# Kernel tuning notes

Measured on AMD Instinct MI355X. Metric: run time of the kernel, lower is better.

Reference implementation:

```python
import jax, jax.numpy as jnp
import numpy as np

OUTCOMES = [8, 8, 8, 8, 8, 8]           # concept outcome counts (concepts_order)
N_TOTAL = int(np.prod(OUTCOMES))        # 262144 joint states
N_VALID = 8192                          # admissible states
B, D = 4096, 1024


def setup_inputs() -> dict:
    key = jax.random.key(0)
    k1, k2 = jax.random.split(key)
    embeddings = jax.random.normal(k1, (B, D), dtype=jnp.float32)
    W = jax.random.normal(k2, (N_VALID, D), dtype=jnp.float32) * 0.02
    b = jnp.zeros((N_VALID,), dtype=jnp.float32)
    # unique sorted admissible-state indices, like torch.argwhere(mask)
    rng = np.random.default_rng(0)
    valid_states = jnp.asarray(
        np.sort(rng.choice(N_TOTAL, size=N_VALID, replace=False)).astype(np.int32))
    return {"embeddings": embeddings, "W": W, "b": b, "valid_states": valid_states}


def reference(embeddings, W, b, valid_states):
    # softmax over valid states: [B, N_VALID]
    probs = jax.nn.softmax(embeddings @ W.T + b, axis=1)
    probs_t = probs.T  # [N_VALID, B] for leading-axis segment reduction
    marginals = []
    stride = N_TOTAL
    for n_i in OUTCOMES:
        stride //= n_i
        # digit of each valid joint-state index along this concept's axis
        digit = (valid_states // stride) % n_i  # [N_VALID]
        # equivalent to scattering probs into the full joint tensor and
        # summing over all other concept axes, without materializing it
        m = jax.ops.segment_sum(probs_t, digit, num_segments=n_i).T  # [B, n_i]
        marginals.append(m)
    return jnp.stack(marginals)  # [n_concepts, B, 8]
```

## Files before the change

kernel.cpp:

```cpp
#include <hip/hip_runtime.h>
#include <hip/hip_bf16.h>
#include <cstdint>
#include <cstddef>

typedef __bf16 bf16_t;
typedef bf16_t bf16x8 __attribute__((ext_vector_type(8)));
typedef bf16_t bf16x4 __attribute__((ext_vector_type(4)));
typedef float  f32x4  __attribute__((ext_vector_type(4)));
typedef unsigned int u32;

#define BROWS 4096
#define NV    8192
#define KD    1024
#define NT    16
#define ST    48
#define LOG2E 1.44269504088896340736f

#define GLL(gsrc, ldst) \
  __builtin_amdgcn_global_load_lds((const __attribute__((address_space(1))) u32*)(gsrc), \
                                   (__attribute__((address_space(3))) u32*)(ldst), 16, 0, 0)
#define FENCE asm volatile("" ::: "memory")

__global__ void cvt_kernel(const float* __restrict__ src, bf16_t* __restrict__ dst, int n4) {
  int idx = blockIdx.x * blockDim.x + threadIdx.x;
  int stride = gridDim.x * blockDim.x;
  for (int i = idx; i < n4; i += stride) {
    float4 v = ((const float4*)src)[i];
    bf16x4 o;
    o[0] = (bf16_t)v.x; o[1] = (bf16_t)v.y; o[2] = (bf16_t)v.z; o[3] = (bf16_t)v.w;
    ((bf16x4*)dst)[i] = o;
  }
}

__global__ void build_s2t_kernel(const int* __restrict__ vstate, bf16_t* __restrict__ s2t) {
  int g = blockIdx.x * blockDim.x + threadIdx.x;
  if (g >= ST * NV) return;
  int b = g >> 13;
  int ig = g & (NV - 1);
  int c = b >> 3;
  int d = b & 7;
  int src = ig ^ ((b & 7) << 3);
  int dig = (vstate[src] >> (15 - 3 * c)) & 7;
  s2t[g] = (bf16_t)(dig == d ? 1.0f : 0.0f);
}

__global__ __launch_bounds__(512, 2)
void gemm_fused_kernel(const bf16_t* __restrict__ W, const bf16_t* __restrict__ E,
                       const float* __restrict__ bias, const bf16_t* __restrict__ s2t,
                       float* __restrict__ part) {
  __shared__ __align__(16) char lds[131072];

  const int t    = threadIdx.x;
  const int lane = t & 63;
  const int wv   = t >> 6;
  const int wm   = wv >> 2;
  const int wn   = wv & 3;
  const int fr   = lane & 15;
  const int fq   = lane >> 4;

  int bid = blockIdx.x;
  int wg  = (bid & 7) * 64 + (bid >> 3);
  const int stile = wg >> 4;
  const int btile = wg & 15;
  const int st0 = stile * 256;
  const int bt0 = btile * 256;

  const int srow = lane >> 2;
  const int skel = ((lane & 3) ^ ((lane >> 3) & 3)) * 8;
  const bf16_t* aptr = W + (size_t)(st0 + wv * 32 + srow) * KD + skel;
  const bf16_t* bptr = E + (size_t)(bt0 + wv * 32 + srow) * KD + skel;
  const int dchunk = (wv * 2) * 1024;

  const int xsw    = (fr & 6) << 3;
  const int a_base = wm * 8192 + ((fr * 64 + fq * 16) ^ xsw);
  const int b_base = wn * 4096 + ((fr * 64 + fq * 16) ^ xsw);

  f32x4 acc[8][4] = {};

  GLL(aptr,                &lds[0 * 16384 + dchunk]);
  GLL(aptr + 16 * KD,      &lds[0 * 16384 + dchunk + 1024]);
  GLL(bptr,                &lds[1 * 16384 + dchunk]);
  GLL(bptr + 16 * KD,      &lds[1 * 16384 + dchunk + 1024]);
  GLL(aptr + 32,           &lds[2 * 16384 + dchunk]);
  GLL(aptr + 32 + 16 * KD, &lds[2 * 16384 + dchunk + 1024]);
  GLL(bptr + 32,           &lds[3 * 16384 + dchunk]);
  GLL(bptr + 32 + 16 * KD, &lds[3 * 16384 + dchunk + 1024]);
  asm volatile("s_waitcnt vmcnt(4)" ::: "memory");
  __builtin_amdgcn_s_barrier();
  FENCE;

  for (int kt = 0; kt < NT; ++kt) {
    const int cb = (kt & 1) * 4;
    const int nb = ((kt + 1) & 1) * 4;
    const char* sA0 = &lds[(cb + 0) * 16384];
    const char* sB0 = &lds[(cb + 1) * 16384];
    const char* sA1 = &lds[(cb + 2) * 16384];
    const char* sB1 = &lds[(cb + 3) * 16384];
    const bool pf = (kt + 1 < NT);
    const int ko = (kt + 1) * 64;

    bf16x8 a[4], b0[4], b1[4];

#pragma unroll
    for (int n = 0; n < 4; ++n)
      b0[n] = *(const bf16x8*)(sB0 + b_base + n * 1024);
#pragma unroll
    for (int mi = 0; mi < 4; ++mi)
      a[mi] = *(const bf16x8*)(sA0 + a_base + mi * 1024);
    if (pf) {
      GLL(aptr + ko,           &lds[(nb + 0) * 16384 + dchunk]);
      GLL(aptr + ko + 16 * KD, &lds[(nb + 0) * 16384 + dchunk + 1024]);
    }
    FENCE; __builtin_amdgcn_s_barrier();
    asm volatile("s_waitcnt lgkmcnt(0)" ::: "memory");
    __builtin_amdgcn_sched_barrier(0);
    __builtin_amdgcn_s_setprio(1);
#pragma unroll
    for (int mi = 0; mi < 4; ++mi)
#pragma unroll
      for (int n = 0; n < 4; ++n)
        acc[mi][n] = __builtin_amdgcn_mfma_f32_16x16x32_bf16(a[mi], b0[n], acc[mi][n], 0, 0, 0);
    __builtin_amdgcn_s_setprio(0);
    FENCE; __builtin_amdgcn_s_barrier(); FENCE;

#pragma unroll
    for (int mi = 0; mi < 4; ++mi)
      a[mi] = *(const bf16x8*)(sA0 + a_base + (4 + mi) * 1024);
    if (pf) {
      GLL(bptr + ko,           &lds[(nb + 1) * 16384 + dchunk]);
      GLL(bptr + ko + 16 * KD, &lds[(nb + 1) * 16384 + dchunk + 1024]);
    }
    FENCE; __builtin_amdgcn_s_barrier();
    asm volatile("s_waitcnt lgkmcnt(0)" ::: "memory");
    __builtin_amdgcn_sched_barrier(0);
    __builtin_amdgcn_s_setprio(1);
#pragma unroll
    for (int mi = 0; mi < 4; ++mi)
#pragma unroll
      for (int n = 0; n < 4; ++n)
        acc[4 + mi][n] = __builtin_amdgcn_mfma_f32_16x16x32_bf16(a[mi], b0[n], acc[4 + mi][n], 0, 0, 0);
    __builtin_amdgcn_s_setprio(0);
    if (pf) asm volatile("s_waitcnt vmcnt(4)" ::: "memory");
    else    asm volatile("s_waitcnt vmcnt(0)" ::: "memory");
    FENCE; __builtin_amdgcn_s_barrier(); FENCE;

#pragma unroll
    for (int n = 0; n < 4; ++n)
      b1[n] = *(const bf16x8*)(sB1 + b_base + n * 1024);
#pragma unroll
    for (int mi = 0; mi < 4; ++mi)
      a[mi] = *(const bf16x8*)(sA1 + a_base + mi * 1024);
    if (pf) {
      GLL(aptr + ko + 32,           &lds[(nb + 2) * 16384 + dchunk]);
      GLL(aptr + ko + 32 + 16 * KD, &lds[(nb + 2) * 16384 + dchunk + 1024]);
    }
    FENCE; __builtin_amdgcn_s_barrier();
    asm volatile("s_waitcnt lgkmcnt(0)" ::: "memory");
    __builtin_amdgcn_sched_barrier(0);
    __builtin_amdgcn_s_setprio(1);
#pragma unroll
    for (int mi = 0; mi < 4; ++mi)
#pragma unroll
      for (int n = 0; n < 4; ++n)
        acc[mi][n] = __builtin_amdgcn_mfma_f32_16x16x32_bf16(a[mi], b1[n], acc[mi][n], 0, 0, 0);
    __builtin_amdgcn_s_setprio(0);
    FENCE; __builtin_amdgcn_s_barrier(); FENCE;

#pragma unroll
    for (int mi = 0; mi < 4; ++mi)
      a[mi] = *(const bf16x8*)(sA1 + a_base + (4 + mi) * 1024);
    if (pf) {
      GLL(bptr + ko + 32,           &lds[(nb + 3) * 16384 + dchunk]);
      GLL(bptr + ko + 32 + 16 * KD, &lds[(nb + 3) * 16384 + dchunk + 1024]);
    }
    FENCE; __builtin_amdgcn_s_barrier();
    asm volatile("s_waitcnt lgkmcnt(0)" ::: "memory");
    __builtin_amdgcn_sched_barrier(0);
    __builtin_amdgcn_s_setprio(1);
#pragma unroll
    for (int mi = 0; mi < 4; ++mi)
#pragma unroll
      for (int n = 0; n < 4; ++n)
        acc[4 + mi][n] = __builtin_amdgcn_mfma_f32_16x16x32_bf16(a[mi], b1[n], acc[4 + mi][n], 0, 0, 0);
    __builtin_amdgcn_s_setprio(0);
    if (pf) asm volatile("s_waitcnt vmcnt(4)" ::: "memory");
    FENCE; __builtin_amdgcn_s_barrier(); FENCE;
  }

  char* const ldsf = &lds[0];
  {
#pragma unroll
    for (int q = 0; q < 3; ++q) {
      const bf16_t* src = s2t + (size_t)(wv * 6 + q * 2 + (lane >> 5)) * NV
                          + st0 + (lane & 31) * 8;
      GLL(src, ldsf + 98304 + wv * 3072 + q * 1024);
    }
  }

  float* const ppart = part + ((size_t)stile * BROWS + bt0) * ST;

#pragma unroll
  for (int pass = 0; pass < 2; ++pass) {
    if ((wn >> 1) == pass) {
#pragma unroll
      for (int m = 0; m < 8; ++m) {
        const float4 bb = *(const float4*)&bias[st0 + wm * 128 + m * 16 + fq * 4];
#pragma unroll
        for (int n = 0; n < 4; ++n) {
          bf16x4 ev;
          ev[0] = (bf16_t)exp2f((acc[m][n][0] + bb.x) * LOG2E);
          ev[1] = (bf16_t)exp2f((acc[m][n][1] + bb.y) * LOG2E);
          ev[2] = (bf16_t)exp2f((acc[m][n][2] + bb.z) * LOG2E);
          ev[3] = (bf16_t)exp2f((acc[m][n][3] + bb.w) * LOG2E);
          const int jh = (wn & 1) * 64 + n * 16 + fr;
          const int ib = (wm * 128 + m * 16 + fq * 4) * 2;
          *(bf16x4*)(ldsf + jh * 512 + (ib ^ ((fr & 7) << 4))) = ev;
        }
      }
    }
    if (pass == 0) asm volatile("s_waitcnt vmcnt(0)" ::: "memory");
    __syncthreads();

    f32x4 acc2[3] = {{0.f,0.f,0.f,0.f},{0.f,0.f,0.f,0.f},{0.f,0.f,0.f,0.f}};
#pragma unroll
    for (int k2 = 0; k2 < 8; ++k2) {
      const int ko2 = (k2 * 64 + fq * 16) ^ ((fr & 7) << 4);
      const bf16x8 ea = *(const bf16x8*)(ldsf + (wv * 16 + fr) * 512 + ko2);
#pragma unroll
      for (int n2 = 0; n2 < 3; ++n2) {
        const bf16x8 sb = *(const bf16x8*)(ldsf + 98304 + (n2 * 16 + fr) * 512 + ko2);
        acc2[n2] = __builtin_amdgcn_mfma_f32_16x16x32_bf16(ea, sb, acc2[n2], 0, 0, 0);
      }
    }
    const int jg = pass * 128 + wv * 16 + fq * 4;
#pragma unroll
    for (int n2 = 0; n2 < 3; ++n2)
#pragma unroll
      for (int r = 0; r < 4; ++r)
        ppart[(size_t)(jg + r) * ST + n2 * 16 + fr] = acc2[n2][r];
    __syncthreads();
  }
}

__global__ __launch_bounds__(64)
void reduce_kernel(const float* __restrict__ part, float* __restrict__ out) {
  const int b = blockIdx.x;
  const int t = threadIdx.x;
  __shared__ float fin[ST];
  if (t < ST) {
    float s = 0.f;
#pragma unroll
    for (int mt = 0; mt < 32; ++mt)
      s += part[((size_t)mt * BROWS + b) * ST + t];
    fin[t] = s;
  }
  __syncthreads();
  if (t < ST) {
    float total = fin[0] + fin[1] + fin[2] + fin[3] + fin[4] + fin[5] + fin[6] + fin[7];
    out[(size_t)(t >> 3) * BROWS * 8 + (size_t)b * 8 + (t & 7)] = fin[t] / total;
  }
}

extern "C" void kernel_launch(void* const* d_in, const int* in_sizes, int n_in,
                              void* d_out, int out_size, void* d_ws, size_t ws_size,
                              hipStream_t stream) {
  const float* E    = (const float*)d_in[0];
  const float* W    = (const float*)d_in[1];
  const float* bias = (const float*)d_in[2];
  const int*   vs   = (const int*)d_in[3];
  float* out = (float*)d_out;

  char* ws = (char*)d_ws;
  size_t off = 0;
  bf16_t* Eb   = (bf16_t*)(ws + off); off += (size_t)BROWS * KD * 2;
  bf16_t* Wb   = (bf16_t*)(ws + off); off += (size_t)NV * KD * 2;
  bf16_t* s2t  = (bf16_t*)(ws + off); off += (size_t)ST * NV * 2;
  float*  part = (float*)(ws + off);  off += (size_t)32 * BROWS * ST * 4;

  build_s2t_kernel<<<(ST * NV + 255) / 256, 256, 0, stream>>>(vs, s2t);
  cvt_kernel<<<2048, 256, 0, stream>>>(E, Eb, BROWS * KD / 4);
  cvt_kernel<<<2048, 256, 0, stream>>>(W, Wb, NV * KD / 4);
  gemm_fused_kernel<<<512, 512, 0, stream>>>(Wb, Eb, bias, s2t, part);
  reduce_kernel<<<BROWS, 64, 0, stream>>>(part, out);
}
```

Measured before the change: 109.3 us.

## Merge conversion kernels, issue prefetch earlier, unroll K loop, transpose partial layout

```diff
diff --git a/kernel.cpp b/kernel.cpp
--- a/kernel.cpp
+++ b/kernel.cpp
@@ -21,14 +21,20 @@
                                    (__attribute__((address_space(3))) u32*)(ldst), 16, 0, 0)
 #define FENCE asm volatile("" ::: "memory")
 
-__global__ void cvt_kernel(const float* __restrict__ src, bf16_t* __restrict__ dst, int n4) {
+__global__ void cvt2_kernel(const float* __restrict__ E, const float* __restrict__ W,
+                            bf16_t* __restrict__ Eb, bf16_t* __restrict__ Wb) {
+  const int nE = BROWS * KD / 4;
+  const int nT = nE + NV * KD / 4;
   int idx = blockIdx.x * blockDim.x + threadIdx.x;
   int stride = gridDim.x * blockDim.x;
-  for (int i = idx; i < n4; i += stride) {
-    float4 v = ((const float4*)src)[i];
+  for (int i = idx; i < nT; i += stride) {
+    const float4* s; bf16x4* d; int j;
+    if (i < nE) { s = (const float4*)E; d = (bf16x4*)Eb; j = i; }
+    else        { s = (const float4*)W; d = (bf16x4*)Wb; j = i - nE; }
+    float4 v = s[j];
     bf16x4 o;
     o[0] = (bf16_t)v.x; o[1] = (bf16_t)v.y; o[2] = (bf16_t)v.z; o[3] = (bf16_t)v.w;
-    ((bf16x4*)dst)[i] = o;
+    d[j] = o;
   }
 }
 
@@ -89,6 +95,7 @@
   __builtin_amdgcn_s_barrier();
   FENCE;
 
+#pragma unroll 2
   for (int kt = 0; kt < NT; ++kt) {
     const int cb = (kt & 1) * 4;
     const int nb = ((kt + 1) & 1) * 4;
@@ -110,26 +117,24 @@
     if (pf) {
       GLL(aptr + ko,           &lds[(nb + 0) * 16384 + dchunk]);
       GLL(aptr + ko + 16 * KD, &lds[(nb + 0) * 16384 + dchunk + 1024]);
-    }
-    FENCE; __builtin_amdgcn_s_barrier();
-    asm volatile("s_waitcnt lgkmcnt(0)" ::: "memory");
-    __builtin_amdgcn_sched_barrier(0);
-    __builtin_amdgcn_s_setprio(1);
-#pragma unroll
-    for (int mi = 0; mi < 4; ++mi)
-#pragma unroll
-      for (int n = 0; n < 4; ++n)
-        acc[mi][n] = __builtin_amdgcn_mfma_f32_16x16x32_bf16(a[mi], b0[n], acc[mi][n], 0, 0, 0);
-    __builtin_amdgcn_s_setprio(0);
-    FENCE; __builtin_amdgcn_s_barrier(); FENCE;
-
-#pragma unroll
-    for (int mi = 0; mi < 4; ++mi)
-      a[mi] = *(const bf16x8*)(sA0 + a_base + (4 + mi) * 1024);
-    if (pf) {
       GLL(bptr + ko,           &lds[(nb + 1) * 16384 + dchunk]);
       GLL(bptr + ko + 16 * KD, &lds[(nb + 1) * 16384 + dchunk + 1024]);
     }
+    FENCE; __builtin_amdgcn_s_barrier();
+    asm volatile("s_waitcnt lgkmcnt(0)" ::: "memory");
+    __builtin_amdgcn_sched_barrier(0);
+    __builtin_amdgcn_s_setprio(1);
+#pragma unroll
+    for (int mi = 0; mi < 4; ++mi)
+#pragma unroll
+      for (int n = 0; n < 4; ++n)
+        acc[mi][n] = __builtin_amdgcn_mfma_f32_16x16x32_bf16(a[mi], b0[n], acc[mi][n], 0, 0, 0);
+    __builtin_amdgcn_s_setprio(0);
+    FENCE; __builtin_amdgcn_s_barrier(); FENCE;
+
+#pragma unroll
+    for (int mi = 0; mi < 4; ++mi)
+      a[mi] = *(const bf16x8*)(sA0 + a_base + (4 + mi) * 1024);
     FENCE; __builtin_amdgcn_s_barrier();
     asm volatile("s_waitcnt lgkmcnt(0)" ::: "memory");
     __builtin_amdgcn_sched_barrier(0);
@@ -153,26 +158,24 @@
     if (pf) {
       GLL(aptr + ko + 32,           &lds[(nb + 2) * 16384 + dchunk]);
       GLL(aptr + ko + 32 + 16 * KD, &lds[(nb + 2) * 16384 + dchunk + 1024]);
-    }
-    FENCE; __builtin_amdgcn_s_barrier();
-    asm volatile("s_waitcnt lgkmcnt(0)" ::: "memory");
-    __builtin_amdgcn_sched_barrier(0);
-    __builtin_amdgcn_s_setprio(1);
-#pragma unroll
-    for (int mi = 0; mi < 4; ++mi)
-#pragma unroll
-      for (int n = 0; n < 4; ++n)
-        acc[mi][n] = __builtin_amdgcn_mfma_f32_16x16x32_bf16(a[mi], b1[n], acc[mi][n], 0, 0, 0);
-    __builtin_amdgcn_s_setprio(0);
-    FENCE; __builtin_amdgcn_s_barrier(); FENCE;
-
-#pragma unroll
-    for (int mi = 0; mi < 4; ++mi)
-      a[mi] = *(const bf16x8*)(sA1 + a_base + (4 + mi) * 1024);
-    if (pf) {
       GLL(bptr + ko + 32,           &lds[(nb + 3) * 16384 + dchunk]);
       GLL(bptr + ko + 32 + 16 * KD, &lds[(nb + 3) * 16384 + dchunk + 1024]);
     }
+    FENCE; __builtin_amdgcn_s_barrier();
+    asm volatile("s_waitcnt lgkmcnt(0)" ::: "memory");
+    __builtin_amdgcn_sched_barrier(0);
+    __builtin_amdgcn_s_setprio(1);
+#pragma unroll
+    for (int mi = 0; mi < 4; ++mi)
+#pragma unroll
+      for (int n = 0; n < 4; ++n)
+        acc[mi][n] = __builtin_amdgcn_mfma_f32_16x16x32_bf16(a[mi], b1[n], acc[mi][n], 0, 0, 0);
+    __builtin_amdgcn_s_setprio(0);
+    FENCE; __builtin_amdgcn_s_barrier(); FENCE;
+
+#pragma unroll
+    for (int mi = 0; mi < 4; ++mi)
+      a[mi] = *(const bf16x8*)(sA1 + a_base + (4 + mi) * 1024);
     FENCE; __builtin_amdgcn_s_barrier();
     asm volatile("s_waitcnt lgkmcnt(0)" ::: "memory");
     __builtin_amdgcn_sched_barrier(0);
@@ -197,7 +200,7 @@
     }
   }
 
-  float* const ppart = part + ((size_t)stile * BROWS + bt0) * ST;
+  float* const ppart = part + (size_t)bt0 * (32 * ST) + (size_t)stile * ST;
 
 #pragma unroll
   for (int pass = 0; pass < 2; ++pass) {
@@ -237,7 +240,7 @@
     for (int n2 = 0; n2 < 3; ++n2)
 #pragma unroll
       for (int r = 0; r < 4; ++r)
-        ppart[(size_t)(jg + r) * ST + n2 * 16 + fr] = acc2[n2][r];
+        ppart[(size_t)(jg + r) * (32 * ST) + n2 * 16 + fr] = acc2[n2][r];
     __syncthreads();
   }
 }
@@ -248,10 +251,11 @@
   const int t = threadIdx.x;
   __shared__ float fin[ST];
   if (t < ST) {
+    const float* p = part + (size_t)b * (32 * ST) + t;
     float s = 0.f;
 #pragma unroll
     for (int mt = 0; mt < 32; ++mt)
-      s += part[((size_t)mt * BROWS + b) * ST + t];
+      s += p[mt * ST];
     fin[t] = s;
   }
   __syncthreads();
@@ -275,11 +279,10 @@
   bf16_t* Eb   = (bf16_t*)(ws + off); off += (size_t)BROWS * KD * 2;
   bf16_t* Wb   = (bf16_t*)(ws + off); off += (size_t)NV * KD * 2;
   bf16_t* s2t  = (bf16_t*)(ws + off); off += (size_t)ST * NV * 2;
-  float*  part = (float*)(ws + off);  off += (size_t)32 * BROWS * ST * 4;
+  float*  part = (float*)(ws + off);  off += (size_t)BROWS * 32 * ST * 4;
 
   build_s2t_kernel<<<(ST * NV + 255) / 256, 256, 0, stream>>>(vs, s2t);
-  cvt_kernel<<<2048, 256, 0, stream>>>(E, Eb, BROWS * KD / 4);
-  cvt_kernel<<<2048, 256, 0, stream>>>(W, Wb, NV * KD / 4);
+  cvt2_kernel<<<3072, 256, 0, stream>>>(E, W, Eb, Wb);
   gemm_fused_kernel<<<512, 512, 0, stream>>>(Wb, Eb, bias, s2t, part);
   reduce_kernel<<<BROWS, 64, 0, stream>>>(part, out);
 }
```

New measurement: 108.0 us. No clear change (-1.2%).
